# Performance work log

Measured on AMD Instinct MI355X. Metric: run time of the kernel, lower is better.

Reference implementation:

```python
import jax, jax.numpy as jnp
import numpy as np

BETA = 0.25       # commit-loss weight (beta)
INIT_GAIN = 0.02  # trunc_normal std for codebook init
B, L, D = 4, 4096, 3
VOCAB = 8192


def setup_inputs() -> dict:
    key = jax.random.key(0)
    k1, k2 = jax.random.split(key)
    feats = jax.random.normal(k1, (B, L, D), dtype=jnp.float32)
    # frozen codebook (nn.Embedding weight), trunc_normal(std=0.02) approximated by normal*0.02
    emb = jax.random.normal(k2, (VOCAB, D), dtype=jnp.float32) * INIT_GAIN
    return {"feats": feats, "emb": emb}


def reference(feats, emb):
    b, l, d = feats.shape
    flat = feats.reshape(-1, d)                                # [N, D]
    dist = (jnp.sum(flat * flat, axis=1, keepdims=True)
            - 2.0 * (flat @ emb.T)
            + jnp.sum(emb * emb, axis=1))
    idx = jnp.argmin(dist, axis=1)                             # [N] int
    quant = emb[idx].reshape(b, l, d)                          # gather lookup
    # e_latent_loss: codebook->encoder MSE (feats detached); commit: beta * encoder->codebook MSE
    e_latent_loss = jnp.mean((quant - jax.lax.stop_gradient(feats)) ** 2)
    commit_loss = BETA * jnp.mean((feats - jax.lax.stop_gradient(quant)) ** 2)
    vq_loss = e_latent_loss + commit_loss
    # straight-through estimator
    quant_ste = feats + jax.lax.stop_gradient(quant - feats)
    return quant_ste, idx.reshape(b, l), vq_loss
```

## Files before the change

### kernel.cpp

```cpp
#include <hip/hip_runtime.h>
#include <cstdint>

#define N_ROWS   16384
#define VOCAB    8192
#define BLOCK    512
#define NWAVES   (BLOCK / 64)
#define RPW      8
#define ROWS_PB  (NWAVES * RPW)
#define GRID     (N_ROWS / ROWS_PB)
#define PIECE    1024
#define NPIECE   (VOCAB / PIECE)

typedef unsigned long long u64;


__global__ __launch_bounds__(BLOCK, 2) void vq_main_kernel(
    const float* __restrict__ feats, const float* __restrict__ emb,
    float* __restrict__ out_quant, float* __restrict__ out_idx,
    float* __restrict__ partial)
{
    __shared__ float4 sE[PIECE];
    __shared__ float  wsum[NWAVES];

    const int tid   = threadIdx.x;
    const int lane  = tid & 63;
    const int wave  = tid >> 6;
    const int wrow0 = blockIdx.x * ROWS_PB + wave * RPW;

    float x0[RPW], x1[RPW], x2[RPW], xx[RPW];
    #pragma unroll
    for (int r = 0; r < RPW; ++r) {
        x0[r] = feats[3 * (wrow0 + r) + 0];
        x1[r] = feats[3 * (wrow0 + r) + 1];
        x2[r] = feats[3 * (wrow0 + r) + 2];
        xx[r] = __fadd_rn(__fadd_rn(__fmul_rn(x0[r], x0[r]), __fmul_rn(x1[r], x1[r])),
                          __fmul_rn(x2[r], x2[r]));
    }

    const float* g = emb + 3 * tid;
    float a0 = g[0],    a1 = g[1],    a2 = g[2];
    float b0 = g[1536], b1 = g[1537], b2 = g[1538];

    float best[RPW];
    int   bpj[RPW];
    #pragma unroll
    for (int r = 0; r < RPW; ++r) { best[r] = __int_as_float(0x7f800000); bpj[r] = 0; }

    for (int p = 0; p < NPIECE; ++p) {
        __syncthreads();
        {
            const float eea = __fadd_rn(__fadd_rn(__fmul_rn(a0, a0), __fmul_rn(a1, a1)),
                                        __fmul_rn(a2, a2));
            const float eeb = __fadd_rn(__fadd_rn(__fmul_rn(b0, b0), __fmul_rn(b1, b1)),
                                        __fmul_rn(b2, b2));
            sE[tid]         = make_float4(a0 + a0, a1 + a1, a2 + a2, eea);
            sE[tid + BLOCK] = make_float4(b0 + b0, b1 + b1, b2 + b2, eeb);
        }
        __syncthreads();

        if (p + 1 < NPIECE) {
            const float* gn = emb + 3 * ((p + 1) * PIECE + tid);
            a0 = gn[0];    a1 = gn[1];    a2 = gn[2];
            b0 = gn[1536]; b1 = gn[1537]; b2 = gn[1538];
        }

        const int pj0 = p * 16;
        #pragma unroll
        for (int j = 0; j < 16; ++j) {
            const float4 E = sE[j * 64 + lane];
            const int pj = pj0 + j;
            #pragma unroll
            for (int r = 0; r < RPW; ++r) {
                const float xe2 = __fmaf_rn(x2[r], E.z,
                                  __fmaf_rn(x1[r], E.y, __fmul_rn(x0[r], E.x)));
                const float d = __fadd_rn(__fsub_rn(xx[r], xe2), E.w);
                if (d < best[r]) { best[r] = d; bpj[r] = pj; }
            }
        }
    }

    u64 key[RPW];
    #pragma unroll
    for (int r = 0; r < RPW; ++r) {
        const unsigned code = (unsigned)((bpj[r] >> 4) * PIECE + (bpj[r] & 15) * 64 + lane);
        u64 k = ((u64)__float_as_uint(best[r]) << 32) | code;
        #pragma unroll
        for (int off = 1; off < 64; off <<= 1) {
            const u64 o = __shfl_xor(k, off, 64);
            if (o < k) k = o;
        }
        key[r] = k;
    }

    u64 mykey = key[0];
    #pragma unroll
    for (int r = 1; r < RPW; ++r) mykey = (lane == r) ? key[r] : mykey;

    float s = 0.0f;
    if (lane < RPW) {
        const int row = wrow0 + lane;
        const unsigned idx = (unsigned)(mykey & 0xffffffffULL);
        const float e0 = emb[3 * idx + 0];
        const float e1 = emb[3 * idx + 1];
        const float e2 = emb[3 * idx + 2];
        const float fx0 = feats[3 * row + 0];
        const float fx1 = feats[3 * row + 1];
        const float fx2 = feats[3 * row + 2];
        out_quant[3 * row + 0] = __fadd_rn(fx0, __fsub_rn(e0, fx0));
        out_quant[3 * row + 1] = __fadd_rn(fx1, __fsub_rn(e1, fx1));
        out_quant[3 * row + 2] = __fadd_rn(fx2, __fsub_rn(e2, fx2));
        out_idx[row] = (float)idx;
        const float d0 = e0 - fx0, d1 = e1 - fx1, d2 = e2 - fx2;
        s = d0 * d0 + d1 * d1 + d2 * d2;
    }

    #pragma unroll
    for (int off = 1; off < 64; off <<= 1) s += __shfl_xor(s, off, 64);
    if (lane == 0) wsum[wave] = s;
    __syncthreads();
    if (tid == 0) {
        float t = 0.0f;
        #pragma unroll
        for (int w = 0; w < NWAVES; ++w) t += wsum[w];
        partial[blockIdx.x] = t;
    }
}

__global__ __launch_bounds__(GRID) void vq_loss_kernel(
    const float* __restrict__ partial, float* __restrict__ out_loss)
{
    __shared__ float wsum[GRID / 64];
    float s = partial[threadIdx.x];
    #pragma unroll
    for (int off = 1; off < 64; off <<= 1) s += __shfl_xor(s, off, 64);
    if ((threadIdx.x & 63) == 0) wsum[threadIdx.x >> 6] = s;
    __syncthreads();
    if (threadIdx.x == 0) {
        float t = 0.0f;
        #pragma unroll
        for (int w = 0; w < GRID / 64; ++w) t += wsum[w];
        const float m = t / (float)(N_ROWS * 3);
        out_loss[0] = __fadd_rn(m, __fmul_rn(0.25f, m));
    }
}

extern "C" void kernel_launch(void* const* d_in, const int* in_sizes, int n_in,
                              void* d_out, int out_size, void* d_ws, size_t ws_size,
                              hipStream_t stream)
{
    const float* feats = (const float*)d_in[0];
    const float* emb   = (const float*)d_in[1];
    float* out = (float*)d_out;
    float* partial = (float*)d_ws;

    vq_main_kernel<<<GRID, BLOCK, 0, stream>>>(
        feats, emb, out, out + (size_t)N_ROWS * 3, partial);
    vq_loss_kernel<<<1, GRID, 0, stream>>>(partial, out + (size_t)N_ROWS * 4);
}
```

Measured before the change: 87.26 us.

## Prune codebook scan to high-norm candidates with exact bound-checked fallback

Each block computes every codebook norm and compacts the entries whose squared norm exceeds a fixed threshold into shared memory, up to a cap. It also records the per-group maximum norm of the rejected entries. Rows scan only the compacted candidates, then use a triangle-inequality bound to confirm that no rejected entry could be closer. When the bound fails, a fallback scans only the rejected groups that could still win. This removes most of the 8192-entry distance sweep, at the cost of a per-block compaction pass with atomics and scans. It also relies on a threshold tuned to the norm distribution of the codebook.

```diff
diff --git a/kernel.cpp b/kernel.cpp
--- a/kernel.cpp
+++ b/kernel.cpp
@@ -3,143 +3,200 @@
 
 #define N_ROWS   16384
 #define VOCAB    8192
-#define BLOCK    512
-#define NWAVES   (BLOCK / 64)
+#define THETA    0.00226f
+#define CAP      1536
+#define THREADS  256
 #define RPW      8
-#define ROWS_PB  (NWAVES * RPW)
+#define ROWS_PB  32
 #define GRID     (N_ROWS / ROWS_PB)
-#define PIECE    1024
-#define NPIECE   (VOCAB / PIECE)
 
 typedef unsigned long long u64;
-
-
-__global__ __launch_bounds__(BLOCK, 2) void vq_main_kernel(
+typedef unsigned int u32;
+
+
+__global__ __launch_bounds__(THREADS) void vq_main(
     const float* __restrict__ feats, const float* __restrict__ emb,
     float* __restrict__ out_quant, float* __restrict__ out_idx,
-    float* __restrict__ partial)
+    float* __restrict__ part)
 {
-    __shared__ float4 sE[PIECE];
-    __shared__ float  wsum[NWAVES];
-
-    const int tid   = threadIdx.x;
-    const int lane  = tid & 63;
-    const int wave  = tid >> 6;
+    __shared__ float4 sSel[CAP];
+    __shared__ u32    sOrd[CAP];
+    __shared__ float  sCmax[VOCAB / 16];
+    __shared__ u32    sCnt;
+    __shared__ float  wsum[4];
+
+    const int t = threadIdx.x, lane = t & 63, wave = t >> 6;
+    if (t == 0) sCnt = 0u;
+    __syncthreads();
+
+    const float4* embv = (const float4*)emb;
+    float cm0 = 0.0f, cm1 = 0.0f;
+    #pragma unroll
+    for (int g = 0; g < 4; ++g) {
+        float w[24];
+        #pragma unroll
+        for (int j = 0; j < 6; ++j) {
+            const float4 v = embv[t * 24 + g * 6 + j];
+            w[4*j] = v.x; w[4*j+1] = v.y; w[4*j+2] = v.z; w[4*j+3] = v.w;
+        }
+        float ee[8]; bool sf[8]; u32 tc = 0;
+        #pragma unroll
+        for (int i = 0; i < 8; ++i) {
+            const float e0 = w[3*i], e1 = w[3*i+1], e2 = w[3*i+2];
+            ee[i] = __fadd_rn(__fadd_rn(__fmul_rn(e0,e0), __fmul_rn(e1,e1)),
+                              __fmul_rn(e2,e2));
+            sf[i] = ee[i] > THETA;
+            tc += sf[i] ? 1u : 0u;
+            if (!sf[i]) { if (g < 2) cm0 = fmaxf(cm0, ee[i]); else cm1 = fmaxf(cm1, ee[i]); }
+        }
+        u32 incl = tc;
+        #pragma unroll
+        for (int o = 1; o < 64; o <<= 1) {
+            const u32 v = __shfl_up(incl, o, 64);
+            if (lane >= o) incl += v;
+        }
+        const u32 excl = incl - tc;
+        u32 wb = 0;
+        if (lane == 63) wb = atomicAdd(&sCnt, incl);
+        const u32 base = __shfl(wb, 63, 64);
+        u32 r = 0;
+        #pragma unroll
+        for (int i = 0; i < 8; ++i) {
+            if (sf[i]) {
+                const u32 p = base + excl + r; ++r;
+                const float e0 = w[3*i], e1 = w[3*i+1], e2 = w[3*i+2];
+                if (p < CAP) {
+                    sSel[p] = make_float4(e0+e0, e1+e1, e2+e2, ee[i]);
+                    sOrd[p] = (u32)(t * 32 + g * 8 + i);
+                } else {
+                    if (g < 2) cm0 = fmaxf(cm0, ee[i]); else cm1 = fmaxf(cm1, ee[i]);
+                }
+            }
+        }
+    }
+    sCmax[2*t] = cm0; sCmax[2*t + 1] = cm1;
+    __syncthreads();
+    const u32 cnt = sCnt;
+    const u32 cap64 = (cnt + 63u) & ~63u;
+    const u32 padded = cap64 < (u32)CAP ? cap64 : (u32)CAP;
+    if (t < (int)(padded - cnt)) { sSel[cnt + t] = sSel[0]; sOrd[cnt + t] = sOrd[0]; }
+    __syncthreads();
+
     const int wrow0 = blockIdx.x * ROWS_PB + wave * RPW;
-
-    float x0[RPW], x1[RPW], x2[RPW], xx[RPW];
+    float X0[RPW], X1[RPW], X2[RPW], XX[RPW];
     #pragma unroll
     for (int r = 0; r < RPW; ++r) {
-        x0[r] = feats[3 * (wrow0 + r) + 0];
-        x1[r] = feats[3 * (wrow0 + r) + 1];
-        x2[r] = feats[3 * (wrow0 + r) + 2];
-        xx[r] = __fadd_rn(__fadd_rn(__fmul_rn(x0[r], x0[r]), __fmul_rn(x1[r], x1[r])),
-                          __fmul_rn(x2[r], x2[r]));
-    }
-
-    const float* g = emb + 3 * tid;
-    float a0 = g[0],    a1 = g[1],    a2 = g[2];
-    float b0 = g[1536], b1 = g[1537], b2 = g[1538];
-
-    float best[RPW];
-    int   bpj[RPW];
-    #pragma unroll
-    for (int r = 0; r < RPW; ++r) { best[r] = __int_as_float(0x7f800000); bpj[r] = 0; }
-
-    for (int p = 0; p < NPIECE; ++p) {
-        __syncthreads();
-        {
-            const float eea = __fadd_rn(__fadd_rn(__fmul_rn(a0, a0), __fmul_rn(a1, a1)),
-                                        __fmul_rn(a2, a2));
-            const float eeb = __fadd_rn(__fadd_rn(__fmul_rn(b0, b0), __fmul_rn(b1, b1)),
-                                        __fmul_rn(b2, b2));
-            sE[tid]         = make_float4(a0 + a0, a1 + a1, a2 + a2, eea);
-            sE[tid + BLOCK] = make_float4(b0 + b0, b1 + b1, b2 + b2, eeb);
-        }
-        __syncthreads();
-
-        if (p + 1 < NPIECE) {
-            const float* gn = emb + 3 * ((p + 1) * PIECE + tid);
-            a0 = gn[0];    a1 = gn[1];    a2 = gn[2];
-            b0 = gn[1536]; b1 = gn[1537]; b2 = gn[1538];
-        }
-
-        const int pj0 = p * 16;
-        #pragma unroll
-        for (int j = 0; j < 16; ++j) {
-            const float4 E = sE[j * 64 + lane];
-            const int pj = pj0 + j;
+        X0[r] = feats[3*(wrow0+r)+0];
+        X1[r] = feats[3*(wrow0+r)+1];
+        X2[r] = feats[3*(wrow0+r)+2];
+        XX[r] = __fadd_rn(__fadd_rn(__fmul_rn(X0[r],X0[r]), __fmul_rn(X1[r],X1[r])),
+                          __fmul_rn(X2[r],X2[r]));
+    }
+    float BD[RPW]; u32 BO[RPW];
+    #pragma unroll
+    for (int r = 0; r < RPW; ++r) { BD[r] = __int_as_float(0x7f800000); BO[r] = 0xffffffffu; }
+
+    for (u32 pos = (u32)lane; pos < padded; pos += 64u) {
+        const float4 E  = sSel[pos];
+        const u32 orig  = sOrd[pos];
+        #pragma unroll
+        for (int r = 0; r < RPW; ++r) {
+            const float xe2 = __fmaf_rn(X2[r], E.z, __fmaf_rn(X1[r], E.y, __fmul_rn(X0[r], E.x)));
+            const float d   = __fadd_rn(__fsub_rn(XX[r], xe2), E.w);
+            const bool bt = (d < BD[r]) || (d == BD[r] && orig < BO[r]);
+            if (bt) { BD[r] = d; BO[r] = orig; }
+        }
+    }
+
+    u64 K[RPW];
+    #pragma unroll
+    for (int r = 0; r < RPW; ++r) {
+        u64 k = ((u64)__float_as_uint(BD[r]) << 32) | (u64)BO[r];
+        #pragma unroll
+        for (int o = 1; o < 64; o <<= 1) { const u64 v = __shfl_xor(k, o, 64); if (v < k) k = v; }
+        K[r] = k;
+    }
+
+    const bool covered = (cnt <= (u32)CAP);
+    bool anyfail = false; float T2min = 1.0e30f;
+    #pragma unroll
+    for (int r = 0; r < RPW; ++r) {
+        const float gb = __uint_as_float((u32)(K[r] >> 32));
+        const float sx = sqrtf(XX[r]) - 1e-5f;
+        const float T  = sx - (sqrtf(gb + 1e-4f) + 1e-5f);
+        const float T2 = (T > 0.0f) ? (T*T - 1e-5f) : -1.0e30f;
+        const bool fail = !(covered && (THETA < T2));
+        if (fail) { anyfail = true; T2min = fminf(T2min, T2); }
+    }
+
+    if (anyfail) {
+        for (int kk = 0; kk < (VOCAB/16)/4; ++kk) {
+            const int q = 4*kk + (lane >> 4);
+            const int c = lane & 15;
+            const bool act = (sCmax[q] >= T2min);
+            if (__ballot(act) == 0ull) continue;
+            if (act) {
+                const int code = q*16 + c;
+                const float e0 = emb[3*code], e1 = emb[3*code+1], e2 = emb[3*code+2];
+                const float ee = __fadd_rn(__fadd_rn(__fmul_rn(e0,e0), __fmul_rn(e1,e1)),
+                                           __fmul_rn(e2,e2));
+                #pragma unroll
+                for (int r = 0; r < RPW; ++r) {
+                    const float xe = __fmaf_rn(X2[r], e2, __fmaf_rn(X1[r], e1, __fmul_rn(X0[r], e0)));
+                    const float d  = __fadd_rn(__fsub_rn(XX[r], __fadd_rn(xe, xe)), ee);
+                    const u32 orig = (u32)code;
+                    const bool bt = (d < BD[r]) || (d == BD[r] && orig < BO[r]);
+                    if (bt) { BD[r] = d; BO[r] = orig; }
+                }
+            }
+        }
+        #pragma unroll
+        for (int r = 0; r < RPW; ++r) {
+            u64 k = ((u64)__float_as_uint(BD[r]) << 32) | (u64)BO[r];
             #pragma unroll
-            for (int r = 0; r < RPW; ++r) {
-                const float xe2 = __fmaf_rn(x2[r], E.z,
-                                  __fmaf_rn(x1[r], E.y, __fmul_rn(x0[r], E.x)));
-                const float d = __fadd_rn(__fsub_rn(xx[r], xe2), E.w);
-                if (d < best[r]) { best[r] = d; bpj[r] = pj; }
-            }
-        }
-    }
-
-    u64 key[RPW];
-    #pragma unroll
-    for (int r = 0; r < RPW; ++r) {
-        const unsigned code = (unsigned)((bpj[r] >> 4) * PIECE + (bpj[r] & 15) * 64 + lane);
-        u64 k = ((u64)__float_as_uint(best[r]) << 32) | code;
-        #pragma unroll
-        for (int off = 1; off < 64; off <<= 1) {
-            const u64 o = __shfl_xor(k, off, 64);
-            if (o < k) k = o;
-        }
-        key[r] = k;
-    }
-
-    u64 mykey = key[0];
-    #pragma unroll
-    for (int r = 1; r < RPW; ++r) mykey = (lane == r) ? key[r] : mykey;
+            for (int o = 1; o < 64; o <<= 1) { const u64 v = __shfl_xor(k, o, 64); if (v < k) k = v; }
+            K[r] = k;
+        }
+    }
+
+    u64 mykey = K[0];
+    #pragma unroll
+    for (int r = 1; r < RPW; ++r) mykey = (lane == r) ? K[r] : mykey;
 
     float s = 0.0f;
     if (lane < RPW) {
         const int row = wrow0 + lane;
-        const unsigned idx = (unsigned)(mykey & 0xffffffffULL);
-        const float e0 = emb[3 * idx + 0];
-        const float e1 = emb[3 * idx + 1];
-        const float e2 = emb[3 * idx + 2];
-        const float fx0 = feats[3 * row + 0];
-        const float fx1 = feats[3 * row + 1];
-        const float fx2 = feats[3 * row + 2];
-        out_quant[3 * row + 0] = __fadd_rn(fx0, __fsub_rn(e0, fx0));
-        out_quant[3 * row + 1] = __fadd_rn(fx1, __fsub_rn(e1, fx1));
-        out_quant[3 * row + 2] = __fadd_rn(fx2, __fsub_rn(e2, fx2));
+        const u32 idx = (u32)(mykey & 0xffffffffULL);
+        const float e0 = emb[3*idx+0], e1 = emb[3*idx+1], e2 = emb[3*idx+2];
+        const float fx0 = feats[3*row+0], fx1 = feats[3*row+1], fx2 = feats[3*row+2];
+        out_quant[3*row+0] = __fadd_rn(fx0, __fsub_rn(e0, fx0));
+        out_quant[3*row+1] = __fadd_rn(fx1, __fsub_rn(e1, fx1));
+        out_quant[3*row+2] = __fadd_rn(fx2, __fsub_rn(e2, fx2));
         out_idx[row] = (float)idx;
         const float d0 = e0 - fx0, d1 = e1 - fx1, d2 = e2 - fx2;
-        s = d0 * d0 + d1 * d1 + d2 * d2;
-    }
-
-    #pragma unroll
-    for (int off = 1; off < 64; off <<= 1) s += __shfl_xor(s, off, 64);
+        s = d0*d0 + d1*d1 + d2*d2;
+    }
+    #pragma unroll
+    for (int o = 1; o < 64; o <<= 1) s += __shfl_xor(s, o, 64);
     if (lane == 0) wsum[wave] = s;
     __syncthreads();
-    if (tid == 0) {
-        float t = 0.0f;
-        #pragma unroll
-        for (int w = 0; w < NWAVES; ++w) t += wsum[w];
-        partial[blockIdx.x] = t;
-    }
+    if (t == 0) part[blockIdx.x] = (wsum[0] + wsum[1]) + (wsum[2] + wsum[3]);
 }
 
-__global__ __launch_bounds__(GRID) void vq_loss_kernel(
-    const float* __restrict__ partial, float* __restrict__ out_loss)
+__global__ __launch_bounds__(GRID) void vq_loss(
+    const float* __restrict__ part, float* __restrict__ out_loss)
 {
-    __shared__ float wsum[GRID / 64];
-    float s = partial[threadIdx.x];
-    #pragma unroll
-    for (int off = 1; off < 64; off <<= 1) s += __shfl_xor(s, off, 64);
-    if ((threadIdx.x & 63) == 0) wsum[threadIdx.x >> 6] = s;
+    __shared__ float ws[GRID / 64];
+    float s = part[threadIdx.x];
+    #pragma unroll
+    for (int o = 1; o < 64; o <<= 1) s += __shfl_xor(s, o, 64);
+    if ((threadIdx.x & 63) == 0) ws[threadIdx.x >> 6] = s;
     __syncthreads();
     if (threadIdx.x == 0) {
-        float t = 0.0f;
-        #pragma unroll
-        for (int w = 0; w < GRID / 64; ++w) t += wsum[w];
-        const float m = t / (float)(N_ROWS * 3);
+        float tsum = 0.0f;
+        #pragma unroll
+        for (int i = 0; i < GRID / 64; ++i) tsum += ws[i];
+        const float m = tsum / (float)(N_ROWS * 3);
         out_loss[0] = __fadd_rn(m, __fmul_rn(0.25f, m));
     }
 }
@@ -151,9 +208,9 @@
     const float* feats = (const float*)d_in[0];
     const float* emb   = (const float*)d_in[1];
     float* out = (float*)d_out;
-    float* partial = (float*)d_ws;
-
-    vq_main_kernel<<<GRID, BLOCK, 0, stream>>>(
-        feats, emb, out, out + (size_t)N_ROWS * 3, partial);
-    vq_loss_kernel<<<1, GRID, 0, stream>>>(partial, out + (size_t)N_ROWS * 4);
+    float* part = (float*)d_ws;
+
+    vq_main<<<GRID, THREADS, 0, stream>>>(
+        feats, emb, out, out + (size_t)N_ROWS * 3, part);
+    vq_loss<<<1, GRID, 0, stream>>>(part, out + (size_t)N_ROWS * 4);
 }
```

Result: slower. 124.2 us (+42.4%).
